# Kernel optimization log

Hardware: AMD Instinct MI355X
Metric: run time of the kernel (lower is better)

## Reference

```python
import jax, jax.numpy as jnp
import numpy as np

N = 100000      # nodes
E = 1600000     # edges
D_IN = 16       # input_dim
D_H = 32        # hidden_dim
D_OUT = 1       # output_dim
N_ITERS = 2
D_CAT = D_H + D_IN          # node feature after cat([H, X])
D_EDGE = 2 * D_CAT          # edge MLP input dim


def setup_inputs() -> dict:
    key = jax.random.key(0)
    ks = jax.random.split(key, 10)
    x = jax.random.normal(ks[0], (N, D_IN), jnp.float32)
    edge_index = jax.random.randint(ks[1], (2, E), 0, N, dtype=jnp.int32)
    # inputnet: Linear(D_IN -> D_H) + Tanh
    W_in = jax.random.normal(ks[2], (D_H, D_IN), jnp.float32) / np.sqrt(D_IN)
    b_in = jnp.zeros((D_H,), jnp.float32)
    # convnn (EdgeConv nn): Linear(D_EDGE -> D_H) + Sigmoid
    W_c = jax.random.normal(ks[3], (D_H, D_EDGE), jnp.float32) / np.sqrt(D_EDGE)
    b_c = jnp.zeros((D_H,), jnp.float32)
    # outputnet: Linear(D_H -> D_OUT) + Sigmoid
    W_out = jax.random.normal(ks[4], (D_OUT, D_H), jnp.float32) / np.sqrt(D_H)
    b_out = jnp.zeros((D_OUT,), jnp.float32)
    return {"x": x, "edge_index": edge_index, "W_in": W_in, "b_in": b_in,
            "W_c": W_c, "b_c": b_c, "W_out": W_out, "b_out": b_out}


def reference(x, edge_index, W_in, b_in, W_c, b_c, W_out, b_out):
    src = edge_index[0]  # x_j (source / neighbor)
    dst = edge_index[1]  # x_i (target, aggregation index)

    H = jnp.tanh(x @ W_in.T + b_in)            # [N, D_H]
    feats = jnp.concatenate([H, x], axis=-1)    # [N, D_CAT]

    for _ in range(N_ITERS):
        xi = feats[dst]                          # [E, D_CAT] gather targets
        xj = feats[src]                          # [E, D_CAT] gather sources
        # PyG EdgeConv message: nn(cat([x_i, x_j - x_i]))
        msg = jax.nn.sigmoid(
            jnp.concatenate([xi, xj - xi], axis=-1) @ W_c.T + b_c)  # [E, D_H]
        H = jax.ops.segment_sum(msg, dst, num_segments=N)           # aggr='add'
        feats = jnp.concatenate([H, x], axis=-1)

    sum_H = jnp.mean(H, axis=0)                  # [D_H]
    return jax.nn.sigmoid(sum_H @ W_out.T + b_out)  # [D_OUT]
```

## Files before the change

kernel.cpp:

```cpp
#include <hip/hip_runtime.h>

#define D_H 32
#define NREP 32
#define SLOTS 48
#define BIN_SHIFT 8
#define MAXNB 512
#define BIN_CAP 5120
#define SB 256


__global__ __launch_bounds__(256) void k_ab0(const float* __restrict__ x,
                      const float* __restrict__ W_in, const float* __restrict__ b_in,
                      const float* __restrict__ W_c, const float* __restrict__ b_c,
                      float* __restrict__ A, float* __restrict__ B, int N) {
    __shared__ float st[32][257];
    int tid = threadIdx.x;
    int n0 = blockIdx.x * 256;
    int n = n0 + tid;
    bool act = n < N;
    float f[48];
    float bbr[32];
    if (act) {
        const float4* xr = (const float4*)(x + (size_t)n * 16);
#pragma unroll
        for (int q = 0; q < 4; ++q) {
            float4 v = xr[q];
            f[32 + 4 * q] = v.x; f[33 + 4 * q] = v.y;
            f[34 + 4 * q] = v.z; f[35 + 4 * q] = v.w;
        }
#pragma unroll
        for (int j = 0; j < 32; ++j) {
            const float* w = W_in + j * 16;
            float acc = b_in[j];
#pragma unroll
            for (int i = 0; i < 16; ++i) acc += f[32 + i] * w[i];
            f[j] = tanhf(acc);
        }
#pragma unroll 4
        for (int j = 0; j < 32; ++j) {
            const float* w = W_c + j * 96;
            float p = b_c[j];
            float bb = 0.f;
#pragma unroll
            for (int i = 0; i < 48; ++i) {
                p  += f[i] * w[i];
                bb += f[i] * w[48 + i];
            }
            st[j][tid] = p - bb;
            bbr[j] = bb;
        }
    }
    __syncthreads();
    float4* A4 = (float4*)(A + (size_t)n0 * D_H);
#pragma unroll
    for (int k = 0; k < 8; ++k) {
        int i4 = k * 256 + tid;
        int nl = i4 >> 3;
        int j0 = (i4 & 7) * 4;
        if (n0 + nl < N) {
            float4 v = {st[j0][nl], st[j0 + 1][nl], st[j0 + 2][nl], st[j0 + 3][nl]};
            A4[i4] = v;
        }
    }
    __syncthreads();
    if (act) {
#pragma unroll
        for (int j = 0; j < 32; ++j) st[j][tid] = bbr[j];
    }
    __syncthreads();
    float4* B4 = (float4*)(B + (size_t)n0 * D_H);
#pragma unroll
    for (int k = 0; k < 8; ++k) {
        int i4 = k * 256 + tid;
        int nl = i4 >> 3;
        int j0 = (i4 & 7) * 4;
        if (n0 + nl < N) {
            float4 v = {st[j0][nl], st[j0 + 1][nl], st[j0 + 2][nl], st[j0 + 3][nl]};
            B4[i4] = v;
        }
    }
}

__global__ __launch_bounds__(256) void k_ab1(const float* __restrict__ H,
                      const float* __restrict__ x, const float* __restrict__ W_c,
                      const float* __restrict__ b_c, float* __restrict__ A,
                      float* __restrict__ B, int N) {
    __shared__ float st[32][257];
    int tid = threadIdx.x;
    int n0 = blockIdx.x * 256;
    int n = n0 + tid;
    bool act = n < N;
    float f[48];
    float bbr[32];
    if (act) {
        const float4* hr = (const float4*)(H + (size_t)n * D_H);
#pragma unroll
        for (int q = 0; q < 8; ++q) {
            float4 v = hr[q];
            f[4 * q]     = v.x; f[4 * q + 1] = v.y;
            f[4 * q + 2] = v.z; f[4 * q + 3] = v.w;
        }
        const float4* xr = (const float4*)(x + (size_t)n * 16);
#pragma unroll
        for (int q = 0; q < 4; ++q) {
            float4 v = xr[q];
            f[32 + 4 * q] = v.x; f[33 + 4 * q] = v.y;
            f[34 + 4 * q] = v.z; f[35 + 4 * q] = v.w;
        }
#pragma unroll 4
        for (int j = 0; j < 32; ++j) {
            const float* w = W_c + j * 96;
            float p = b_c[j];
            float bb = 0.f;
#pragma unroll
            for (int i = 0; i < 48; ++i) {
                p  += f[i] * w[i];
                bb += f[i] * w[48 + i];
            }
            st[j][tid] = p - bb;
            bbr[j] = bb;
        }
    }
    __syncthreads();
    float4* A4 = (float4*)(A + (size_t)n0 * D_H);
#pragma unroll
    for (int k = 0; k < 8; ++k) {
        int i4 = k * 256 + tid;
        int nl = i4 >> 3;
        int j0 = (i4 & 7) * 4;
        if (n0 + nl < N) {
            float4 v = {st[j0][nl], st[j0 + 1][nl], st[j0 + 2][nl], st[j0 + 3][nl]};
            A4[i4] = v;
        }
    }
    __syncthreads();
    if (act) {
#pragma unroll
        for (int j = 0; j < 32; ++j) st[j][tid] = bbr[j];
    }
    __syncthreads();
    float4* B4 = (float4*)(B + (size_t)n0 * D_H);
#pragma unroll
    for (int k = 0; k < 8; ++k) {
        int i4 = k * 256 + tid;
        int nl = i4 >> 3;
        int j0 = (i4 & 7) * 4;
        if (n0 + nl < N) {
            float4 v = {st[j0][nl], st[j0 + 1][nl], st[j0 + 2][nl], st[j0 + 3][nl]};
            B4[i4] = v;
        }
    }
}

__global__ __launch_bounds__(256) void k_bin(const int* __restrict__ src,
                                             const int* __restrict__ dst,
                                             int* __restrict__ binCnt,
                                             unsigned int* __restrict__ ebuf, int E) {
    __shared__ int hist[MAXNB];
    int tid = threadIdx.x;
    for (int i = tid; i < MAXNB; i += 256) hist[i] = 0;
    __syncthreads();
    int chunk = (E + SB - 1) / SB;
    int lo = blockIdx.x * chunk;
    int hi = lo + chunk; if (hi > E) hi = E;
    for (int e = lo + tid; e < hi; e += 256) {
        int b = dst[e] >> BIN_SHIFT;
        atomicAdd(&hist[b], 1);
    }
    __syncthreads();
    for (int b = tid; b < MAXNB; b += 256) {
        int c = hist[b];
        int base = c ? atomicAdd(&binCnt[b], c) : 0;
        hist[b] = b * BIN_CAP + base;
    }
    __syncthreads();
    for (int e = lo + tid; e < hi; e += 256) {
        int d = dst[e];
        int s = src[e];
        int b = d >> BIN_SHIFT;
        int pos = atomicAdd(&hist[b], 1);
        if ((unsigned)(pos - b * BIN_CAP) < (unsigned)BIN_CAP)
            ebuf[pos] = ((unsigned)(d & 255) << 24) | (unsigned)s;
    }
}

__global__ __launch_bounds__(256) void k_place(const int* __restrict__ binCnt,
                                               const unsigned int* __restrict__ ebuf,
                                               int* __restrict__ ssrcp,
                                               int* __restrict__ cntG, int N) {
    __shared__ int cnt[256];
    int tid = threadIdx.x;
    int w = blockIdx.x;
    cnt[tid] = 0;
    __syncthreads();
    int n = binCnt[w]; if (n > BIN_CAP) n = BIN_CAP;
    int base = w * BIN_CAP;
    for (int j = tid; j < n; j += 256) {
        unsigned int v = ebuf[base + j];
        int ld = v >> 24;
        int s = v & 0xFFFFFF;
        int slot = atomicAdd(&cnt[ld], 1);
        if (slot < SLOTS)
            ssrcp[(size_t)((w << BIN_SHIFT) + ld) * SLOTS + slot] = s;
    }
    __syncthreads();
    int node = (w << BIN_SHIFT) + tid;
    if (node < N) cntG[node] = cnt[tid] < SLOTS ? cnt[tid] : SLOTS;
}


__global__ void k_gather1(const int* __restrict__ cntG, const int* __restrict__ ssrcp,
                          const float* __restrict__ A, const float* __restrict__ B,
                          float* __restrict__ H, int N) {
    int t = blockIdx.x * blockDim.x + threadIdx.x;
    int d = t >> 5;
    if (d >= N) return;
    int l = t & 31;
    int q = l & 7;
    int s = l >> 3;
    int len = cntG[d];
    const int* base = ssrcp + (size_t)d * SLOTS;
    float4 a4 = ((const float4*)(A + (size_t)d * D_H))[q];
    float4 acc = {0.f, 0.f, 0.f, 0.f};
    int j = s;
    for (; j + 4 < len; j += 8) {
        int s0 = base[j], s1 = base[j + 4];
        float4 b0 = ((const float4*)(B + (size_t)s0 * D_H))[q];
        float4 b1 = ((const float4*)(B + (size_t)s1 * D_H))[q];
        acc.x += 1.f / (1.f + __expf(-(a4.x + b0.x)));
        acc.y += 1.f / (1.f + __expf(-(a4.y + b0.y)));
        acc.z += 1.f / (1.f + __expf(-(a4.z + b0.z)));
        acc.w += 1.f / (1.f + __expf(-(a4.w + b0.w)));
        acc.x += 1.f / (1.f + __expf(-(a4.x + b1.x)));
        acc.y += 1.f / (1.f + __expf(-(a4.y + b1.y)));
        acc.z += 1.f / (1.f + __expf(-(a4.z + b1.z)));
        acc.w += 1.f / (1.f + __expf(-(a4.w + b1.w)));
    }
    if (j < len) {
        int s0 = base[j];
        float4 b0 = ((const float4*)(B + (size_t)s0 * D_H))[q];
        acc.x += 1.f / (1.f + __expf(-(a4.x + b0.x)));
        acc.y += 1.f / (1.f + __expf(-(a4.y + b0.y)));
        acc.z += 1.f / (1.f + __expf(-(a4.z + b0.z)));
        acc.w += 1.f / (1.f + __expf(-(a4.w + b0.w)));
    }
    acc.x += __shfl_xor(acc.x, 8);  acc.y += __shfl_xor(acc.y, 8);
    acc.z += __shfl_xor(acc.z, 8);  acc.w += __shfl_xor(acc.w, 8);
    acc.x += __shfl_xor(acc.x, 16); acc.y += __shfl_xor(acc.y, 16);
    acc.z += __shfl_xor(acc.z, 16); acc.w += __shfl_xor(acc.w, 16);
    if (s == 0) ((float4*)(H + (size_t)d * D_H))[q] = acc;
}

__global__ void k_gather2(const int* __restrict__ cntG, const int* __restrict__ ssrcp,
                          const float* __restrict__ A, const float* __restrict__ B,
                          float* __restrict__ Srep, int N) {
    int l = threadIdx.x & 31;
    int slot = threadIdx.x >> 5;
    int q = l & 7;
    int s = l >> 3;
    int d = blockIdx.x * 8 + slot;
    float4 acc = {0.f, 0.f, 0.f, 0.f};
    if (d < N) {
        int len = cntG[d];
        const int* base = ssrcp + (size_t)d * SLOTS;
        float4 a4 = ((const float4*)(A + (size_t)d * D_H))[q];
        int j = s;
        for (; j + 4 < len; j += 8) {
            int s0 = base[j], s1 = base[j + 4];
            float4 b0 = ((const float4*)(B + (size_t)s0 * D_H))[q];
            float4 b1 = ((const float4*)(B + (size_t)s1 * D_H))[q];
            acc.x += 1.f / (1.f + __expf(-(a4.x + b0.x)));
            acc.y += 1.f / (1.f + __expf(-(a4.y + b0.y)));
            acc.z += 1.f / (1.f + __expf(-(a4.z + b0.z)));
            acc.w += 1.f / (1.f + __expf(-(a4.w + b0.w)));
            acc.x += 1.f / (1.f + __expf(-(a4.x + b1.x)));
            acc.y += 1.f / (1.f + __expf(-(a4.y + b1.y)));
            acc.z += 1.f / (1.f + __expf(-(a4.z + b1.z)));
            acc.w += 1.f / (1.f + __expf(-(a4.w + b1.w)));
        }
        if (j < len) {
            int s0 = base[j];
            float4 b0 = ((const float4*)(B + (size_t)s0 * D_H))[q];
            acc.x += 1.f / (1.f + __expf(-(a4.x + b0.x)));
            acc.y += 1.f / (1.f + __expf(-(a4.y + b0.y)));
            acc.z += 1.f / (1.f + __expf(-(a4.z + b0.z)));
            acc.w += 1.f / (1.f + __expf(-(a4.w + b0.w)));
        }
    }
    acc.x += __shfl_xor(acc.x, 8);  acc.y += __shfl_xor(acc.y, 8);
    acc.z += __shfl_xor(acc.z, 8);  acc.w += __shfl_xor(acc.w, 8);
    acc.x += __shfl_xor(acc.x, 16); acc.y += __shfl_xor(acc.y, 16);
    acc.z += __shfl_xor(acc.z, 16); acc.w += __shfl_xor(acc.w, 16);
    __shared__ float red[8][32];
    if (s == 0) {
        red[slot][4 * q + 0] = acc.x;
        red[slot][4 * q + 1] = acc.y;
        red[slot][4 * q + 2] = acc.z;
        red[slot][4 * q + 3] = acc.w;
    }
    __syncthreads();
    if (threadIdx.x < 32) {
        float sm = 0.f;
#pragma unroll
        for (int r = 0; r < 8; ++r) sm += red[r][threadIdx.x];
        unsafeAtomicAdd(&Srep[(blockIdx.x & (NREP - 1)) * D_H + threadIdx.x], sm);
    }
}

__global__ void k_final(const float* __restrict__ Srep, const float* __restrict__ W_out,
                        const float* __restrict__ b_out, float* __restrict__ out,
                        float invN) {
    int j = threadIdx.x;
    float v = 0.f;
    if (j < 32) {
        float s = 0.f;
#pragma unroll
        for (int r = 0; r < NREP; ++r) s += Srep[r * D_H + j];
        v = s * invN * W_out[j];
    }
#pragma unroll
    for (int off = 32; off > 0; off >>= 1) v += __shfl_down(v, off);
    if (j == 0) out[0] = 1.f / (1.f + __expf(-(v + b_out[0])));
}

extern "C" void kernel_launch(void* const* d_in, const int* in_sizes, int n_in,
                              void* d_out, int out_size, void* d_ws, size_t ws_size,
                              hipStream_t stream) {
    const float* x     = (const float*)d_in[0];
    const int*   ei    = (const int*)d_in[1];
    const float* W_in  = (const float*)d_in[2];
    const float* b_in  = (const float*)d_in[3];
    const float* W_c   = (const float*)d_in[4];
    const float* b_c   = (const float*)d_in[5];
    const float* W_out = (const float*)d_in[6];
    const float* b_out = (const float*)d_in[7];

    const int N = in_sizes[0] / 16;
    const int E = in_sizes[1] / 2;
    const int* src = ei;
    const int* dst = ei + E;

    const int NB = (N + 255) >> BIN_SHIFT;

    float* H    = (float*)d_ws;
    float* A    = H + (size_t)N * D_H;
    float* B    = A + (size_t)N * D_H;
    float* Srep = B + (size_t)N * D_H;
    int*   cntG   = (int*)(Srep + NREP * D_H);
    int*   binCnt = cntG + N;
    int*   ssrcp  = binCnt + MAXNB;
    unsigned int* ebuf = (unsigned int*)A;

    float* out = (float*)d_out;

    hipMemsetAsync(binCnt, 0, MAXNB * sizeof(int), stream);
    k_bin<<<SB, 256, 0, stream>>>(src, dst, binCnt, ebuf, E);
    k_place<<<NB, 256, 0, stream>>>(binCnt, ebuf, ssrcp, cntG, N);

    k_ab0<<<(N + 255) / 256, 256, 0, stream>>>(x, W_in, b_in, W_c, b_c, A, B, N);
    k_gather1<<<(int)(((size_t)N * 32 + 255) / 256), 256, 0, stream>>>(cntG, ssrcp, A, B, H, N);

    k_ab1<<<(N + 255) / 256, 256, 0, stream>>>(H, x, W_c, b_c, A, B, N);
    hipMemsetAsync(Srep, 0, NREP * D_H * sizeof(float), stream);
    k_gather2<<<(N + 7) / 8, 256, 0, stream>>>(cntG, ssrcp, A, B, Srep, N);

    k_final<<<1, 64, 0, stream>>>(Srep, W_out, b_out, out, 1.f / (float)N);
}
```

Measured before the change: 275.3 us.

## Fuse node-projection and edge-binning into one launch; split output features across half-blocks

```diff
diff --git a/kernel.cpp b/kernel.cpp
--- a/kernel.cpp
+++ b/kernel.cpp
@@ -7,20 +7,139 @@
 #define MAXNB 512
 #define BIN_CAP 5120
 #define SB 256
-
-
-__global__ __launch_bounds__(256) void k_ab0(const float* __restrict__ x,
-                      const float* __restrict__ W_in, const float* __restrict__ b_in,
-                      const float* __restrict__ W_c, const float* __restrict__ b_c,
-                      float* __restrict__ A, float* __restrict__ B, int N) {
-    __shared__ float st[32][257];
+#define AB_NPB 128
+
+
+__global__ __launch_bounds__(256) void k_ab0bin(
+        const float* __restrict__ x, const float* __restrict__ W_in,
+        const float* __restrict__ b_in, const float* __restrict__ W_c,
+        const float* __restrict__ b_c, float* __restrict__ A, float* __restrict__ B,
+        int N, int abBlocks,
+        const int* __restrict__ src, const int* __restrict__ dst,
+        int* __restrict__ binCnt, unsigned int* __restrict__ ebuf, int E) {
+    __shared__ float st[32][AB_NPB + 1];
     int tid = threadIdx.x;
-    int n0 = blockIdx.x * 256;
-    int n = n0 + tid;
+    int bid = blockIdx.x;
+
+    if (bid < abBlocks) {
+        int n0 = bid * AB_NPB;
+        int nl = tid & (AB_NPB - 1);
+        int half = tid >> 7;
+        int n = n0 + nl;
+        bool act = n < N;
+        float f[48];
+        float bbr[16];
+        if (act) {
+            const float4* xr = (const float4*)(x + (size_t)n * 16);
+#pragma unroll
+            for (int q = 0; q < 4; ++q) {
+                float4 v = xr[q];
+                f[32 + 4 * q] = v.x; f[33 + 4 * q] = v.y;
+                f[34 + 4 * q] = v.z; f[35 + 4 * q] = v.w;
+            }
+#pragma unroll
+            for (int j = 0; j < 32; ++j) {
+                const float* w = W_in + j * 16;
+                float acc = b_in[j];
+#pragma unroll
+                for (int i = 0; i < 16; ++i) acc += f[32 + i] * w[i];
+                f[j] = tanhf(acc);
+            }
+#pragma unroll 4
+            for (int jj = 0; jj < 16; ++jj) {
+                int j = half * 16 + jj;
+                const float* w = W_c + j * 96;
+                float p = b_c[j];
+                float bb = 0.f;
+#pragma unroll
+                for (int i = 0; i < 48; ++i) {
+                    p  += f[i] * w[i];
+                    bb += f[i] * w[48 + i];
+                }
+                st[j][nl] = p - bb;
+                bbr[jj] = bb;
+            }
+        }
+        __syncthreads();
+        float4* A4 = (float4*)(A + (size_t)n0 * D_H);
+#pragma unroll
+        for (int k = 0; k < 4; ++k) {
+            int i4 = k * 256 + tid;
+            int nn = i4 >> 3;
+            int j0 = (i4 & 7) * 4;
+            if (n0 + nn < N) {
+                float4 v = {st[j0][nn], st[j0 + 1][nn], st[j0 + 2][nn], st[j0 + 3][nn]};
+                A4[i4] = v;
+            }
+        }
+        __syncthreads();
+        if (act) {
+#pragma unroll
+            for (int jj = 0; jj < 16; ++jj) st[half * 16 + jj][nl] = bbr[jj];
+        }
+        __syncthreads();
+        float4* B4 = (float4*)(B + (size_t)n0 * D_H);
+#pragma unroll
+        for (int k = 0; k < 4; ++k) {
+            int i4 = k * 256 + tid;
+            int nn = i4 >> 3;
+            int j0 = (i4 & 7) * 4;
+            if (n0 + nn < N) {
+                float4 v = {st[j0][nn], st[j0 + 1][nn], st[j0 + 2][nn], st[j0 + 3][nn]};
+                B4[i4] = v;
+            }
+        }
+    } else {
+        int* hist = (int*)st;
+        int b0 = bid - abBlocks;
+        for (int i = tid; i < MAXNB; i += 256) hist[i] = 0;
+        __syncthreads();
+        int chunk = (E + SB - 1) / SB;
+        int lo = b0 * chunk;
+        int hi = lo + chunk; if (hi > E) hi = E;
+        for (int e = lo + tid; e < hi; e += 256) {
+            int b = dst[e] >> BIN_SHIFT;
+            atomicAdd(&hist[b], 1);
+        }
+        __syncthreads();
+        for (int b = tid; b < MAXNB; b += 256) {
+            int c = hist[b];
+            int base = c ? atomicAdd(&binCnt[b], c) : 0;
+            hist[b] = b * BIN_CAP + base;
+        }
+        __syncthreads();
+        for (int e = lo + tid; e < hi; e += 256) {
+            int d = dst[e];
+            int s = src[e];
+            int b = d >> BIN_SHIFT;
+            int pos = atomicAdd(&hist[b], 1);
+            if ((unsigned)(pos - b * BIN_CAP) < (unsigned)BIN_CAP)
+                ebuf[pos] = ((unsigned)(d & 255) << 24) | (unsigned)s;
+        }
+    }
+}
+
+__global__ __launch_bounds__(256) void k_ab1(const float* __restrict__ H,
+                      const float* __restrict__ x, const float* __restrict__ W_c,
+                      const float* __restrict__ b_c, float* __restrict__ A,
+                      float* __restrict__ B, int N) {
+    __shared__ float st[32][AB_NPB + 1];
+    int tid = threadIdx.x;
+    int n0 = blockIdx.x * AB_NPB;
+    int nl = tid & (AB_NPB - 1);
+    int half = tid >> 7;
+    int n = n0 + nl;
     bool act = n < N;
     float f[48];
-    float bbr[32];
+    float bbr[16];
     if (act) {
+        const float4* hr = (const float4*)(H + (size_t)n * D_H);
+#pragma unroll
+        for (int q = 0; q < 8; ++q) {
+            float4 v = hr[q];
+            f[4 * q]     = v.x; f[4 * q + 1] = v.y;
+            f[4 * q + 2] = v.z; f[4 * q + 3] = v.w;
+        }
         const float4* xr = (const float4*)(x + (size_t)n * 16);
 #pragma unroll
         for (int q = 0; q < 4; ++q) {
@@ -28,16 +147,9 @@
             f[32 + 4 * q] = v.x; f[33 + 4 * q] = v.y;
             f[34 + 4 * q] = v.z; f[35 + 4 * q] = v.w;
         }
-#pragma unroll
-        for (int j = 0; j < 32; ++j) {
-            const float* w = W_in + j * 16;
-            float acc = b_in[j];
-#pragma unroll
-            for (int i = 0; i < 16; ++i) acc += f[32 + i] * w[i];
-            f[j] = tanhf(acc);
-        }
 #pragma unroll 4
-        for (int j = 0; j < 32; ++j) {
+        for (int jj = 0; jj < 16; ++jj) {
+            int j = half * 16 + jj;
             const float* w = W_c + j * 96;
             float p = b_c[j];
             float bb = 0.f;
@@ -46,141 +158,38 @@
                 p  += f[i] * w[i];
                 bb += f[i] * w[48 + i];
             }
-            st[j][tid] = p - bb;
-            bbr[j] = bb;
+            st[j][nl] = p - bb;
+            bbr[jj] = bb;
         }
     }
     __syncthreads();
     float4* A4 = (float4*)(A + (size_t)n0 * D_H);
 #pragma unroll
-    for (int k = 0; k < 8; ++k) {
+    for (int k = 0; k < 4; ++k) {
         int i4 = k * 256 + tid;
-        int nl = i4 >> 3;
+        int nn = i4 >> 3;
         int j0 = (i4 & 7) * 4;
-        if (n0 + nl < N) {
-            float4 v = {st[j0][nl], st[j0 + 1][nl], st[j0 + 2][nl], st[j0 + 3][nl]};
+        if (n0 + nn < N) {
+            float4 v = {st[j0][nn], st[j0 + 1][nn], st[j0 + 2][nn], st[j0 + 3][nn]};
             A4[i4] = v;
         }
     }
     __syncthreads();
     if (act) {
 #pragma unroll
-        for (int j = 0; j < 32; ++j) st[j][tid] = bbr[j];
+        for (int jj = 0; jj < 16; ++jj) st[half * 16 + jj][nl] = bbr[jj];
     }
     __syncthreads();
     float4* B4 = (float4*)(B + (size_t)n0 * D_H);
 #pragma unroll
-    for (int k = 0; k < 8; ++k) {
+    for (int k = 0; k < 4; ++k) {
         int i4 = k * 256 + tid;
-        int nl = i4 >> 3;
+        int nn = i4 >> 3;
         int j0 = (i4 & 7) * 4;
-        if (n0 + nl < N) {
-            float4 v = {st[j0][nl], st[j0 + 1][nl], st[j0 + 2][nl], st[j0 + 3][nl]};
+        if (n0 + nn < N) {
+            float4 v = {st[j0][nn], st[j0 + 1][nn], st[j0 + 2][nn], st[j0 + 3][nn]};
             B4[i4] = v;
         }
-    }
-}
-
-__global__ __launch_bounds__(256) void k_ab1(const float* __restrict__ H,
-                      const float* __restrict__ x, const float* __restrict__ W_c,
-                      const float* __restrict__ b_c, float* __restrict__ A,
-                      float* __restrict__ B, int N) {
-    __shared__ float st[32][257];
-    int tid = threadIdx.x;
-    int n0 = blockIdx.x * 256;
-    int n = n0 + tid;
-    bool act = n < N;
-    float f[48];
-    float bbr[32];
-    if (act) {
-        const float4* hr = (const float4*)(H + (size_t)n * D_H);
-#pragma unroll
-        for (int q = 0; q < 8; ++q) {
-            float4 v = hr[q];
-            f[4 * q]     = v.x; f[4 * q + 1] = v.y;
-            f[4 * q + 2] = v.z; f[4 * q + 3] = v.w;
-        }
-        const float4* xr = (const float4*)(x + (size_t)n * 16);
-#pragma unroll
-        for (int q = 0; q < 4; ++q) {
-            float4 v = xr[q];
-            f[32 + 4 * q] = v.x; f[33 + 4 * q] = v.y;
-            f[34 + 4 * q] = v.z; f[35 + 4 * q] = v.w;
-        }
-#pragma unroll 4
-        for (int j = 0; j < 32; ++j) {
-            const float* w = W_c + j * 96;
-            float p = b_c[j];
-            float bb = 0.f;
-#pragma unroll
-            for (int i = 0; i < 48; ++i) {
-                p  += f[i] * w[i];
-                bb += f[i] * w[48 + i];
-            }
-            st[j][tid] = p - bb;
-            bbr[j] = bb;
-        }
-    }
-    __syncthreads();
-    float4* A4 = (float4*)(A + (size_t)n0 * D_H);
-#pragma unroll
-    for (int k = 0; k < 8; ++k) {
-        int i4 = k * 256 + tid;
-        int nl = i4 >> 3;
-        int j0 = (i4 & 7) * 4;
-        if (n0 + nl < N) {
-            float4 v = {st[j0][nl], st[j0 + 1][nl], st[j0 + 2][nl], st[j0 + 3][nl]};
-            A4[i4] = v;
-        }
-    }
-    __syncthreads();
-    if (act) {
-#pragma unroll
-        for (int j = 0; j < 32; ++j) st[j][tid] = bbr[j];
-    }
-    __syncthreads();
-    float4* B4 = (float4*)(B + (size_t)n0 * D_H);
-#pragma unroll
-    for (int k = 0; k < 8; ++k) {
-        int i4 = k * 256 + tid;
-        int nl = i4 >> 3;
-        int j0 = (i4 & 7) * 4;
-        if (n0 + nl < N) {
-            float4 v = {st[j0][nl], st[j0 + 1][nl], st[j0 + 2][nl], st[j0 + 3][nl]};
-            B4[i4] = v;
-        }
-    }
-}
-
-__global__ __launch_bounds__(256) void k_bin(const int* __restrict__ src,
-                                             const int* __restrict__ dst,
-                                             int* __restrict__ binCnt,
-                                             unsigned int* __restrict__ ebuf, int E) {
-    __shared__ int hist[MAXNB];
-    int tid = threadIdx.x;
-    for (int i = tid; i < MAXNB; i += 256) hist[i] = 0;
-    __syncthreads();
-    int chunk = (E + SB - 1) / SB;
-    int lo = blockIdx.x * chunk;
-    int hi = lo + chunk; if (hi > E) hi = E;
-    for (int e = lo + tid; e < hi; e += 256) {
-        int b = dst[e] >> BIN_SHIFT;
-        atomicAdd(&hist[b], 1);
-    }
-    __syncthreads();
-    for (int b = tid; b < MAXNB; b += 256) {
-        int c = hist[b];
-        int base = c ? atomicAdd(&binCnt[b], c) : 0;
-        hist[b] = b * BIN_CAP + base;
-    }
-    __syncthreads();
-    for (int e = lo + tid; e < hi; e += 256) {
-        int d = dst[e];
-        int s = src[e];
-        int b = d >> BIN_SHIFT;
-        int pos = atomicAdd(&hist[b], 1);
-        if ((unsigned)(pos - b * BIN_CAP) < (unsigned)BIN_CAP)
-            ebuf[pos] = ((unsigned)(d & 255) << 24) | (unsigned)s;
     }
 }
 
@@ -349,18 +358,20 @@
     int*   cntG   = (int*)(Srep + NREP * D_H);
     int*   binCnt = cntG + N;
     int*   ssrcp  = binCnt + MAXNB;
-    unsigned int* ebuf = (unsigned int*)A;
+    unsigned int* ebuf = (unsigned int*)H;
 
     float* out = (float*)d_out;
 
+    const int abBlocks = (N + AB_NPB - 1) / AB_NPB;
+
     hipMemsetAsync(binCnt, 0, MAXNB * sizeof(int), stream);
-    k_bin<<<SB, 256, 0, stream>>>(src, dst, binCnt, ebuf, E);
+    k_ab0bin<<<abBlocks + SB, 256, 0, stream>>>(x, W_in, b_in, W_c, b_c, A, B,
+                                                N, abBlocks, src, dst, binCnt, ebuf, E);
     k_place<<<NB, 256, 0, stream>>>(binCnt, ebuf, ssrcp, cntG, N);
 
-    k_ab0<<<(N + 255) / 256, 256, 0, stream>>>(x, W_in, b_in, W_c, b_c, A, B, N);
     k_gather1<<<(int)(((size_t)N * 32 + 255) / 256), 256, 0, stream>>>(cntG, ssrcp, A, B, H, N);
 
-    k_ab1<<<(N + 255) / 256, 256, 0, stream>>>(H, x, W_c, b_c, A, B, N);
+    k_ab1<<<abBlocks, 256, 0, stream>>>(H, x, W_c, b_c, A, B, N);
     hipMemsetAsync(Srep, 0, NREP * D_H * sizeof(float), stream);
     k_gather2<<<(N + 7) / 8, 256, 0, stream>>>(cntG, ssrcp, A, B, Srep, N);
 
```

New measurement: 326.3 us. +18.5%, slower.
